# Optimization experiments

Measured on AMD Instinct MI355X. Metric: run time of the kernel, lower is better.

Reference implementation:

```python
import jax, jax.numpy as jnp
import numpy as np

E = 8        # n_routed_experts
K = 4        # num_experts_per_tok
T = 1024     # tokens
H = 1024     # hidden_size
I = 1408     # moe_intermediate_size


def setup_inputs() -> dict:
    key = jax.random.key(0)
    ks = jax.random.split(key, 6)
    hidden_states = jax.random.normal(ks[0], (T, H), jnp.float32)
    rw = jax.random.uniform(ks[1], (T, K), jnp.float32)
    router_weights = rw / jnp.sum(rw, axis=-1, keepdims=True)  # normalized top-k router weights
    selected_experts = jax.random.randint(ks[2], (T, K), 0, E, jnp.int32)
    gate_w = jax.random.normal(ks[3], (E, H, I), jnp.float32) * (H ** -0.5)  # lecun_normal-ish
    up_w = jax.random.normal(ks[4], (E, H, I), jnp.float32) * (H ** -0.5)
    down_w = jax.random.normal(ks[5], (E, I, H), jnp.float32) * (I ** -0.5)
    return {
        'hidden_states': hidden_states,
        'router_weights': router_weights,
        'gate_w': gate_w,
        'up_w': up_w,
        'down_w': down_w,
        'selected_experts': selected_experts,
    }


def _grouped_matmul(x, w, seg):
    # x: [m, k] tokens sorted by expert; w: [E, k, n]; seg: [m] expert id per row.
    # Grouped GEMM expressed as E masked GEMMs (fixed small loop over experts);
    # a custom kernel would do true variable-group-size grouped GEMM.
    out = jnp.zeros((x.shape[0], w.shape[-1]), x.dtype)
    for e in range(w.shape[0]):
        out = out + jnp.where((seg == e)[:, None], x, jnp.zeros((), x.dtype)) @ w[e]
    return out


def reference(hidden_states, router_weights, gate_w, up_w, down_w, selected_experts):
    t, k = selected_experts.shape
    flat = selected_experts.ravel()                       # [t*k]
    hs = jnp.repeat(hidden_states, k, axis=0)             # [t*k, H]
    sort_idx = jnp.argsort(flat)                          # dispatch: sort tokens by expert
    seg = flat[sort_idx]
    xs = hs[sort_idx]
    gate = _grouped_matmul(xs, gate_w, seg)               # [t*k, I]
    up = _grouped_matmul(xs, up_w, seg)                   # [t*k, I]
    h = jax.nn.silu(gate) * up                            # fused SwiGLU
    down = _grouped_matmul(h, down_w, seg)                # [t*k, H]
    unsort = jnp.argsort(sort_idx)                        # scatter back to token order
    out = down[unsort].reshape(t, k, -1)
    return jnp.sum(out * router_weights[..., None], axis=1)  # weighted combine [t, H]
```

## Files before the change

### kernel.cpp

```cpp
#include <hip/hip_runtime.h>
#include <hip/hip_bf16.h>
#include <cstdint>
#include <cstddef>

#define NE 8
#define NT 1024
#define NK 4
#define NH 1024
#define NI 1408
#define NA (NT * NK)
#define BM 128
#define MAXTILES 40
#define PADSLOTS 5120

typedef short short8 __attribute__((ext_vector_type(8)));
typedef float f32x4 __attribute__((ext_vector_type(4)));
typedef float f4v __attribute__((ext_vector_type(4)));
typedef unsigned short u16;

#define WS_HDR   0
#define WS_SORT  1024
#define WS_XBF   21504
#define WS_GT    2118656
#define WS_UT    25187328
#define WS_DT    48256000
#define WS_HB    71324672

__device__ __forceinline__ u16 f2b(float f) {
  union { float f; uint32_t u; } c; c.f = f;
  uint32_t u = c.u;
  return (u16)((u + 0x7FFFu + ((u >> 16) & 1u)) >> 16);
}

__device__ __forceinline__ void llds16(const void* g, void* l) {
  __builtin_amdgcn_global_load_lds(
      (const __attribute__((address_space(1))) void*)g,
      (__attribute__((address_space(3))) void*)l, 16, 0, 0);
}

__device__ __forceinline__ void transcvt_stripe(const float* __restrict__ src,
                                                u16* __restrict__ dst,
                                                int K, int N, int k0, int n0,
                                                u16* smem, int tid) {
  u16 (*t2)[64][72] = (u16(*)[64][72])smem;
  int r = tid >> 4, c = tid & 15;
  f4v v[2][4];
#pragma unroll
  for (int t = 0; t < 2; ++t)
#pragma unroll
    for (int i = 0; i < 4; ++i)
      v[t][i] = __builtin_nontemporal_load(
          (const f4v*)&src[(size_t)(k0 + r + 16 * i) * N + n0 + t * 64 + c * 4]);
#pragma unroll
  for (int t = 0; t < 2; ++t)
#pragma unroll
    for (int i = 0; i < 4; ++i) {
      ushort4 o;
      o.x = f2b(v[t][i].x); o.y = f2b(v[t][i].y); o.z = f2b(v[t][i].z); o.w = f2b(v[t][i].w);
      *(ushort4*)&t2[t][r + 16 * i][c * 4] = o;
    }
  __syncthreads();
#pragma unroll
  for (int t = 0; t < 2; ++t)
#pragma unroll
    for (int i = 0; i < 2; ++i) {
      int idx = i * 256 + tid;
      int n = idx >> 3, kc = idx & 7;
      u16 o[8];
#pragma unroll
      for (int j = 0; j < 8; ++j) o[j] = t2[t][kc * 8 + j][n];
      *(short8*)&dst[(size_t)(n0 + t * 64 + n) * K + k0 + kc * 8] = *(const short8*)o;
    }
}

__global__ __launch_bounds__(256) void k1_prep(
    const float* __restrict__ gw, const float* __restrict__ uw, const float* __restrict__ dw,
    const float* __restrict__ hs, const int* __restrict__ sel,
    u16* __restrict__ gT, u16* __restrict__ uT, u16* __restrict__ dT, u16* __restrict__ xbf,
    int* __restrict__ hdr, int* __restrict__ sorted, float* __restrict__ outz) {
  int tid = threadIdx.x;
  int y = blockIdx.y;
  if (y == 24) {
    for (int i = blockIdx.x * 256 + tid; i * 4 < NT * NH; i += 176 * 256) {
      f4v v = __builtin_nontemporal_load((const f4v*)&hs[i * 4]);
      ushort4 o;
      o.x = f2b(v.x); o.y = f2b(v.y); o.z = f2b(v.z); o.w = f2b(v.w);
      *(ushort4*)&xbf[i * 4] = o;
    }
    return;
  }
  if (y == 25) {
    int x = blockIdx.x;
    if (x >= 1 && x <= 64) {
      int base = (x - 1) * 16384;
      f4v z = {0.f, 0.f, 0.f, 0.f};
#pragma unroll
      for (int i = 0; i < 16; ++i)
        *(f4v*)&outz[base + (i * 256 + tid) * 4] = z;
      return;
    }
    if (x != 0) return;
    __shared__ int cnt[NE], fill[NE], poff_s[NE + 1];
    if (tid < NE) { cnt[tid] = 0; fill[tid] = 0; }
    __syncthreads();
    for (int i = tid; i < NA; i += 256) atomicAdd(&cnt[sel[i]], 1);
    __syncthreads();
    if (tid == 0) {
      int off = 0, nt = 0;
      for (int e = 0; e < NE; ++e) {
        poff_s[e] = off;
        int tiles = (cnt[e] + BM - 1) / BM;
        for (int j = 0; j < tiles; ++j) { hdr[32 + nt] = e; hdr[80 + nt] = off + j * BM; ++nt; }
        off += tiles * BM;
      }
      poff_s[NE] = off;
      hdr[17] = nt;
      for (int e = 0; e < NE; ++e) hdr[e] = cnt[e];
      for (int e = 0; e <= NE; ++e) hdr[8 + e] = poff_s[e];
    }
    __syncthreads();
    for (int i = tid; i < PADSLOTS; i += 256) sorted[i] = -1;
    __syncthreads();
    for (int i = tid; i < NA; i += 256) {
      int e = sel[i];
      int p = atomicAdd(&fill[e], 1);
      sorted[poff_s[e] + p] = i;
    }
    return;
  }
  __shared__ u16 smem[2 * 64 * 72];
  if (y < 16) {
    int tensor = y >> 3, e = y & 7;
    const float* src = ((tensor == 0) ? gw : uw) + (size_t)e * NH * NI;
    u16* dst = ((tensor == 0) ? gT : uT) + (size_t)e * NH * NI;
    int nb = blockIdx.x % 11, kb = blockIdx.x / 11;
    transcvt_stripe(src, dst, NH, NI, kb * 64, nb * 128, smem, tid);
  } else {
    int e = y - 16;
    const float* src = dw + (size_t)e * NI * NH;
    u16* dst = dT + (size_t)e * NI * NH;
    int nb = blockIdx.x % 8, kb = blockIdx.x / 8;
    transcvt_stripe(src, dst, NI, NH, kb * 64, nb * 128, smem, tid);
  }
}

__global__ __launch_bounds__(256, 2) void k2_gemm1(
    const u16* __restrict__ xbf, const u16* __restrict__ gT, const u16* __restrict__ uT,
    u16* __restrict__ hbuf, const int* __restrict__ hdr, const int* __restrict__ sorted) {
  __shared__ u16 smem[24576];
  int b = blockIdx.x;
  int tid = threadIdx.x;

  int tile = b % 40;
  if (tile >= hdr[17]) return;
  int e = hdr[32 + tile];
  int slot0 = hdr[80 + tile];
  int n0 = (b / 40) * 128;

  u16* sA  = smem;
  u16* sBg = smem + 8192;
  u16* sBu = smem + 16384;

  const u16* aptr[4];
  for (int s = 0; s < 4; ++s) {
    int idx = s * 256 + tid;
    int row = idx >> 3, c = idx & 7;
    int kc = c ^ (row & 7);
    int as = sorted[slot0 + row];
    int trow = (as >= 0) ? (as >> 2) : 0;
    aptr[s] = xbf + (size_t)trow * NH + kc * 8;
  }
  const u16 *bgp[4], *bup[4];
  for (int s = 0; s < 4; ++s) {
    int idx = s * 256 + tid;
    int n = idx >> 3, c = idx & 7;
    int kc = c ^ (n & 7);
    size_t o = ((size_t)e * NI + n0 + n) * NH + kc * 8;
    bgp[s] = gT + o; bup[s] = uT + o;
  }

  int lane = tid & 63, wave = tid >> 6;
  int wm = wave >> 1, wn = wave & 1;
  int l15 = lane & 15, quad = lane >> 4;
  int sw = l15 & 7;

  f32x4 accg[4][4] = {}; f32x4 accu[4][4] = {};

  for (int kt = 0; kt < NH / 64; ++kt) {
    int ko = kt * 64;
    for (int s = 0; s < 4; ++s) llds16(aptr[s] + ko, &sA[(s * 256 + tid) * 8]);
    for (int s = 0; s < 4; ++s) llds16(bgp[s] + ko, &sBg[(s * 256 + tid) * 8]);
    for (int s = 0; s < 4; ++s) llds16(bup[s] + ko, &sBu[(s * 256 + tid) * 8]);
    __syncthreads();
    for (int ks = 0; ks < 2; ++ks) {
      int pos = ((ks * 4 + quad) ^ sw) * 8;
      short8 av[4], bg[4], bu[4];
      for (int mf = 0; mf < 4; ++mf)
        av[mf] = *(const short8*)&sA[(wm * 64 + mf * 16 + l15) * 64 + pos];
      for (int nf = 0; nf < 4; ++nf) {
        bg[nf] = *(const short8*)&sBg[(wn * 64 + nf * 16 + l15) * 64 + pos];
        bu[nf] = *(const short8*)&sBu[(wn * 64 + nf * 16 + l15) * 64 + pos];
      }
      for (int mf = 0; mf < 4; ++mf)
        for (int nf = 0; nf < 4; ++nf) {
          accg[mf][nf] = __builtin_amdgcn_mfma_f32_16x16x32_bf16(av[mf], bg[nf], accg[mf][nf], 0, 0, 0);
          accu[mf][nf] = __builtin_amdgcn_mfma_f32_16x16x32_bf16(av[mf], bu[nf], accu[mf][nf], 0, 0, 0);
        }
    }
    __syncthreads();
  }

  for (int mf = 0; mf < 4; ++mf)
    for (int nf = 0; nf < 4; ++nf)
      for (int r = 0; r < 4; ++r) {
        int row = wm * 64 + mf * 16 + quad * 4 + r;
        int col = n0 + wn * 64 + nf * 16 + l15;
        float g2 = accg[mf][nf][r], u = accu[mf][nf][r];
        float hv = (g2 / (1.f + __expf(-g2))) * u;
        hbuf[(size_t)(slot0 + row) * NI + col] = f2b(hv);
      }
}

__global__ __launch_bounds__(256, 4) void k3_gemm2(
    const u16* __restrict__ hbuf, const u16* __restrict__ dT,
    const float* __restrict__ rw, float* __restrict__ out,
    const int* __restrict__ hdr, const int* __restrict__ sorted) {
  int tile = blockIdx.x;
  if (tile >= hdr[17]) return;
  int e = hdr[32 + tile];
  int slot0 = hdr[80 + tile];
  int n0 = blockIdx.y * 128;
  int tid = threadIdx.x;

  __shared__ u16 sA[128 * 64];
  __shared__ u16 sB[128 * 64];

  const u16 *ap[4], *bp[4];
  for (int s = 0; s < 4; ++s) {
    int idx = s * 256 + tid;
    int r = idx >> 3, c = idx & 7;
    int kc = c ^ (r & 7);
    ap[s] = hbuf + (size_t)(slot0 + r) * NI + kc * 8;
    bp[s] = dT + ((size_t)e * NH + n0 + r) * NI + kc * 8;
  }

  int lane = tid & 63, wave = tid >> 6;
  int wm = wave >> 1, wn = wave & 1;
  int l15 = lane & 15, quad = lane >> 4;
  int sw = l15 & 7;

  f32x4 acc[4][4] = {};

  for (int kt = 0; kt < NI / 64; ++kt) {
    int ko = kt * 64;
    for (int s = 0; s < 4; ++s) llds16(ap[s] + ko, &sA[(s * 256 + tid) * 8]);
    for (int s = 0; s < 4; ++s) llds16(bp[s] + ko, &sB[(s * 256 + tid) * 8]);
    __syncthreads();
    for (int ks = 0; ks < 2; ++ks) {
      int pos = ((ks * 4 + quad) ^ sw) * 8;
      short8 av[4], bv[4];
      for (int mf = 0; mf < 4; ++mf)
        av[mf] = *(const short8*)&sA[(wm * 64 + mf * 16 + l15) * 64 + pos];
      for (int nf = 0; nf < 4; ++nf)
        bv[nf] = *(const short8*)&sB[(wn * 64 + nf * 16 + l15) * 64 + pos];
      for (int mf = 0; mf < 4; ++mf)
        for (int nf = 0; nf < 4; ++nf)
          acc[mf][nf] = __builtin_amdgcn_mfma_f32_16x16x32_bf16(av[mf], bv[nf], acc[mf][nf], 0, 0, 0);
    }
    __syncthreads();
  }

  for (int mf = 0; mf < 4; ++mf) {
    int rowb = wm * 64 + mf * 16 + quad * 4;
    for (int r = 0; r < 4; ++r) {
      int as = sorted[slot0 + rowb + r];
      if (as < 0) continue;
      float w = rw[as];
      float* orow = out + (size_t)(as >> 2) * NH + n0 + wn * 64;
      for (int nf = 0; nf < 4; ++nf)
        atomicAdd(&orow[nf * 16 + l15], w * acc[mf][nf][r]);
    }
  }
}

extern "C" void kernel_launch(void* const* d_in, const int* in_sizes, int n_in,
                              void* d_out, int out_size, void* d_ws, size_t ws_size,
                              hipStream_t stream) {
  const float* hs  = (const float*)d_in[0];
  const float* rw  = (const float*)d_in[1];
  const float* gw  = (const float*)d_in[2];
  const float* uw  = (const float*)d_in[3];
  const float* dw  = (const float*)d_in[4];
  const int*   sel = (const int*)d_in[5];
  float* out = (float*)d_out;

  char* ws = (char*)d_ws;
  int*  hdr    = (int*)(ws + WS_HDR);
  int*  sorted = (int*)(ws + WS_SORT);
  u16*  xbf    = (u16*)(ws + WS_XBF);
  u16*  gT     = (u16*)(ws + WS_GT);
  u16*  uT     = (u16*)(ws + WS_UT);
  u16*  dT     = (u16*)(ws + WS_DT);
  u16*  hb     = (u16*)(ws + WS_HB);

  hipLaunchKernelGGL(k1_prep, dim3(176, 26), dim3(256), 0, stream,
                     gw, uw, dw, hs, sel, gT, uT, dT, xbf, hdr, sorted, out);
  hipLaunchKernelGGL(k2_gemm1, dim3(440), dim3(256), 0, stream,
                     xbf, gT, uT, hb, hdr, sorted);
  hipLaunchKernelGGL(k3_gemm2, dim3(MAXTILES, NH / 128), dim3(256), 0, stream,
                     hb, dT, rw, out, hdr, sorted);
}
```

Before: 243.7 us.

## Overlap down-weight transpose-convert with first grouped GEMM and shrink LDS stride

Moves the down_w fp32-to-bf16 transpose from the prep kernel into extra blocks of the gate/up GEMM kernel, so that conversion can run alongside the first GEMM instead of before it. The prep grid shrinks accordingly. The LDS transpose tile stride also changes from 72 to 66 to alter bank mapping. Risks include the extra blocks competing with GEMM blocks for CUs and bandwidth, and the odd stride possibly misaligning the ushort4 LDS stores.

```diff
diff --git a/kernel.cpp b/kernel.cpp
--- a/kernel.cpp
+++ b/kernel.cpp
@@ -26,6 +26,8 @@
 #define WS_DT    48256000
 #define WS_HB    71324672
 
+#define TSTRIDE 66
+
 __device__ __forceinline__ u16 f2b(float f) {
   union { float f; uint32_t u; } c; c.f = f;
   uint32_t u = c.u;
@@ -42,7 +44,7 @@
                                                 u16* __restrict__ dst,
                                                 int K, int N, int k0, int n0,
                                                 u16* smem, int tid) {
-  u16 (*t2)[64][72] = (u16(*)[64][72])smem;
+  u16 (*t2)[64][TSTRIDE] = (u16(*)[64][TSTRIDE])smem;
   int r = tid >> 4, c = tid & 15;
   f4v v[2][4];
 #pragma unroll
@@ -74,13 +76,13 @@
 }
 
 __global__ __launch_bounds__(256) void k1_prep(
-    const float* __restrict__ gw, const float* __restrict__ uw, const float* __restrict__ dw,
+    const float* __restrict__ gw, const float* __restrict__ uw,
     const float* __restrict__ hs, const int* __restrict__ sel,
-    u16* __restrict__ gT, u16* __restrict__ uT, u16* __restrict__ dT, u16* __restrict__ xbf,
+    u16* __restrict__ gT, u16* __restrict__ uT, u16* __restrict__ xbf,
     int* __restrict__ hdr, int* __restrict__ sorted, float* __restrict__ outz) {
   int tid = threadIdx.x;
   int y = blockIdx.y;
-  if (y == 24) {
+  if (y == 16) {
     for (int i = blockIdx.x * 256 + tid; i * 4 < NT * NH; i += 176 * 256) {
       f4v v = __builtin_nontemporal_load((const f4v*)&hs[i * 4]);
       ushort4 o;
@@ -89,7 +91,7 @@
     }
     return;
   }
-  if (y == 25) {
+  if (y == 17) {
     int x = blockIdx.x;
     if (x >= 1 && x <= 64) {
       int base = (x - 1) * 16384;
@@ -128,28 +130,30 @@
     }
     return;
   }
-  __shared__ u16 smem[2 * 64 * 72];
-  if (y < 16) {
-    int tensor = y >> 3, e = y & 7;
-    const float* src = ((tensor == 0) ? gw : uw) + (size_t)e * NH * NI;
-    u16* dst = ((tensor == 0) ? gT : uT) + (size_t)e * NH * NI;
-    int nb = blockIdx.x % 11, kb = blockIdx.x / 11;
-    transcvt_stripe(src, dst, NH, NI, kb * 64, nb * 128, smem, tid);
-  } else {
-    int e = y - 16;
-    const float* src = dw + (size_t)e * NI * NH;
-    u16* dst = dT + (size_t)e * NI * NH;
-    int nb = blockIdx.x % 8, kb = blockIdx.x / 8;
-    transcvt_stripe(src, dst, NI, NH, kb * 64, nb * 128, smem, tid);
-  }
+  __shared__ u16 smem[2 * 64 * TSTRIDE];
+  int tensor = y >> 3, e = y & 7;
+  const float* src = ((tensor == 0) ? gw : uw) + (size_t)e * NH * NI;
+  u16* dst = ((tensor == 0) ? gT : uT) + (size_t)e * NH * NI;
+  int nb = blockIdx.x % 11, kb = blockIdx.x / 11;
+  transcvt_stripe(src, dst, NH, NI, kb * 64, nb * 128, smem, tid);
 }
 
 __global__ __launch_bounds__(256, 2) void k2_gemm1(
     const u16* __restrict__ xbf, const u16* __restrict__ gT, const u16* __restrict__ uT,
-    u16* __restrict__ hbuf, const int* __restrict__ hdr, const int* __restrict__ sorted) {
+    u16* __restrict__ hbuf, const int* __restrict__ hdr, const int* __restrict__ sorted,
+    const float* __restrict__ dw, u16* __restrict__ dT) {
   __shared__ u16 smem[24576];
   int b = blockIdx.x;
   int tid = threadIdx.x;
+
+  if (b >= 440) {
+    int bb = b - 440;
+    int e = bb / 176, x = bb % 176;
+    int nb = x % 8, kb = x / 8;
+    transcvt_stripe(dw + (size_t)e * NI * NH, dT + (size_t)e * NI * NH,
+                    NI, NH, kb * 64, nb * 128, smem, tid);
+    return;
+  }
 
   int tile = b % 40;
   if (tile >= hdr[17]) return;
@@ -303,10 +307,10 @@
   u16*  dT     = (u16*)(ws + WS_DT);
   u16*  hb     = (u16*)(ws + WS_HB);
 
-  hipLaunchKernelGGL(k1_prep, dim3(176, 26), dim3(256), 0, stream,
-                     gw, uw, dw, hs, sel, gT, uT, dT, xbf, hdr, sorted, out);
-  hipLaunchKernelGGL(k2_gemm1, dim3(440), dim3(256), 0, stream,
-                     xbf, gT, uT, hb, hdr, sorted);
+  hipLaunchKernelGGL(k1_prep, dim3(176, 18), dim3(256), 0, stream,
+                     gw, uw, hs, sel, gT, uT, xbf, hdr, sorted, out);
+  hipLaunchKernelGGL(k2_gemm1, dim3(440 + 1408), dim3(256), 0, stream,
+                     xbf, gT, uT, hb, hdr, sorted, dw, dT);
   hipLaunchKernelGGL(k3_gemm2, dim3(MAXTILES, NH / 128), dim3(256), 0, stream,
                      hb, dT, rw, out, hdr, sorted);
 }
```

Measured after the change: 245.6 us. About the same (+0.8%).

## Pair expert tiles into 256-row blocks with double-buffered LDS and split-K down GEMM

Applied to the files above, without the earlier changes.

Groups consecutive 128-row tiles of the same expert into pairs so each 1024-thread block computes 256 rows, sharing each weight tile load across twice as many tokens. Both GEMMs now double-buffer LDS stages so the next K slice loads during MFMA work, and the down projection splits K in two halves that combine through the existing atomic adds. The transpose scratch stride also changes from 72 to 66. This cuts weight traffic and load latency exposure at the cost of fewer, larger blocks, more LDS per block, and twice the atomics in the second GEMM.

```diff
diff --git a/kernel.cpp b/kernel.cpp
--- a/kernel.cpp
+++ b/kernel.cpp
@@ -11,6 +11,7 @@
 #define NA (NT * NK)
 #define BM 128
 #define MAXTILES 40
+#define MAXPAIRS 24
 #define PADSLOTS 5120
 
 typedef short short8 __attribute__((ext_vector_type(8)));
@@ -26,6 +27,8 @@
 #define WS_DT    48256000
 #define WS_HB    71324672
 
+#define TSTRIDE 66
+
 __device__ __forceinline__ u16 f2b(float f) {
   union { float f; uint32_t u; } c; c.f = f;
   uint32_t u = c.u;
@@ -42,7 +45,7 @@
                                                 u16* __restrict__ dst,
                                                 int K, int N, int k0, int n0,
                                                 u16* smem, int tid) {
-  u16 (*t2)[64][72] = (u16(*)[64][72])smem;
+  u16 (*t2)[64][TSTRIDE] = (u16(*)[64][TSTRIDE])smem;
   int r = tid >> 4, c = tid & 15;
   f4v v[2][4];
 #pragma unroll
@@ -106,15 +109,21 @@
     for (int i = tid; i < NA; i += 256) atomicAdd(&cnt[sel[i]], 1);
     __syncthreads();
     if (tid == 0) {
-      int off = 0, nt = 0;
+      int off = 0, nt = 0, np = 0;
       for (int e = 0; e < NE; ++e) {
         poff_s[e] = off;
         int tiles = (cnt[e] + BM - 1) / BM;
         for (int j = 0; j < tiles; ++j) { hdr[32 + nt] = e; hdr[80 + nt] = off + j * BM; ++nt; }
+        for (int j = 0; j < tiles; j += 2) {
+          hdr[128 + np] = e;
+          hdr[160 + np] = off + j * BM;
+          hdr[192 + np] = (j + 1 < tiles) ? (off + (j + 1) * BM) : -1;
+          ++np;
+        }
         off += tiles * BM;
       }
       poff_s[NE] = off;
-      hdr[17] = nt;
+      hdr[17] = nt; hdr[18] = np;
       for (int e = 0; e < NE; ++e) hdr[e] = cnt[e];
       for (int e = 0; e <= NE; ++e) hdr[8 + e] = poff_s[e];
     }
@@ -128,7 +137,7 @@
     }
     return;
   }
-  __shared__ u16 smem[2 * 64 * 72];
+  __shared__ u16 smem[2 * 64 * TSTRIDE];
   if (y < 16) {
     int tensor = y >> 3, e = y & 7;
     const float* src = ((tensor == 0) ? gw : uw) + (size_t)e * NH * NI;
@@ -144,65 +153,76 @@
   }
 }
 
-__global__ __launch_bounds__(256, 2) void k2_gemm1(
+__global__ __launch_bounds__(1024, 4) void k2_gemm1(
     const u16* __restrict__ xbf, const u16* __restrict__ gT, const u16* __restrict__ uT,
     u16* __restrict__ hbuf, const int* __restrict__ hdr, const int* __restrict__ sorted) {
-  __shared__ u16 smem[24576];
+  __shared__ u16 smem[65536];
   int b = blockIdx.x;
+  int p = b / 11, n0 = (b % 11) * 128;
+  if (p >= hdr[18]) return;
+  int e = hdr[128 + p], slotA = hdr[160 + p], slotB = hdr[192 + p];
   int tid = threadIdx.x;
 
-  int tile = b % 40;
-  if (tile >= hdr[17]) return;
-  int e = hdr[32 + tile];
-  int slot0 = hdr[80 + tile];
-  int n0 = (b / 40) * 128;
-
-  u16* sA  = smem;
-  u16* sBg = smem + 8192;
-  u16* sBu = smem + 16384;
-
-  const u16* aptr[4];
-  for (int s = 0; s < 4; ++s) {
-    int idx = s * 256 + tid;
+  const u16* aptr[2];
+#pragma unroll
+  for (int s = 0; s < 2; ++s) {
+    int idx = s * 1024 + tid;
     int row = idx >> 3, c = idx & 7;
     int kc = c ^ (row & 7);
-    int as = sorted[slot0 + row];
+    int srow = (row < 128) ? (slotA + row) : (slotB >= 0 ? slotB + row - 128 : 0);
+    int as = sorted[srow];
     int trow = (as >= 0) ? (as >> 2) : 0;
     aptr[s] = xbf + (size_t)trow * NH + kc * 8;
   }
-  const u16 *bgp[4], *bup[4];
-  for (int s = 0; s < 4; ++s) {
-    int idx = s * 256 + tid;
-    int n = idx >> 3, c = idx & 7;
-    int kc = c ^ (n & 7);
-    size_t o = ((size_t)e * NI + n0 + n) * NH + kc * 8;
-    bgp[s] = gT + o; bup[s] = uT + o;
-  }
+  {
+  }
+  int bn = tid >> 3, bc = tid & 7;
+  int bkc = bc ^ (bn & 7);
+  size_t bo = ((size_t)e * NI + n0 + bn) * NH + bkc * 8;
+  const u16* bgp = gT + bo;
+  const u16* bup = uT + bo;
 
   int lane = tid & 63, wave = tid >> 6;
-  int wm = wave >> 1, wn = wave & 1;
+  int wm = wave >> 2, wn = wave & 3;
   int l15 = lane & 15, quad = lane >> 4;
   int sw = l15 & 7;
 
-  f32x4 accg[4][4] = {}; f32x4 accu[4][4] = {};
-
-  for (int kt = 0; kt < NH / 64; ++kt) {
-    int ko = kt * 64;
-    for (int s = 0; s < 4; ++s) llds16(aptr[s] + ko, &sA[(s * 256 + tid) * 8]);
-    for (int s = 0; s < 4; ++s) llds16(bgp[s] + ko, &sBg[(s * 256 + tid) * 8]);
-    for (int s = 0; s < 4; ++s) llds16(bup[s] + ko, &sBu[(s * 256 + tid) * 8]);
-    __syncthreads();
+  f32x4 accg[4][2] = {}; f32x4 accu[4][2] = {};
+
+#define K2_STAGE(BUF, KT)                                                     \
+  {                                                                           \
+    int ko_ = (KT) * 64;                                                      \
+    u16* base_ = smem + (BUF) * 32768;                                        \
+    llds16(aptr[0] + ko_, base_ + tid * 8);                                   \
+    llds16(aptr[1] + ko_, base_ + (1024 + tid) * 8);                          \
+    llds16(bgp + ko_, base_ + 16384 + tid * 8);                               \
+    llds16(bup + ko_, base_ + 24576 + tid * 8);                               \
+  }
+
+  K2_STAGE(0, 0);
+  __syncthreads();
+  for (int kt = 0; kt < 16; ++kt) {
+    int cur = kt & 1;
+    if (kt < 15) K2_STAGE(cur ^ 1, kt + 1);
+    const u16* sA  = smem + cur * 32768;
+    const u16* sBg = sA + 16384;
+    const u16* sBu = sA + 24576;
+#pragma unroll
     for (int ks = 0; ks < 2; ++ks) {
       int pos = ((ks * 4 + quad) ^ sw) * 8;
-      short8 av[4], bg[4], bu[4];
+      short8 av[4], bg[2], bu[2];
+#pragma unroll
       for (int mf = 0; mf < 4; ++mf)
         av[mf] = *(const short8*)&sA[(wm * 64 + mf * 16 + l15) * 64 + pos];
-      for (int nf = 0; nf < 4; ++nf) {
-        bg[nf] = *(const short8*)&sBg[(wn * 64 + nf * 16 + l15) * 64 + pos];
-        bu[nf] = *(const short8*)&sBu[(wn * 64 + nf * 16 + l15) * 64 + pos];
+#pragma unroll
+      for (int nf = 0; nf < 2; ++nf) {
+        bg[nf] = *(const short8*)&sBg[(wn * 32 + nf * 16 + l15) * 64 + pos];
+        bu[nf] = *(const short8*)&sBu[(wn * 32 + nf * 16 + l15) * 64 + pos];
       }
+#pragma unroll
       for (int mf = 0; mf < 4; ++mf)
-        for (int nf = 0; nf < 4; ++nf) {
+#pragma unroll
+        for (int nf = 0; nf < 2; ++nf) {
           accg[mf][nf] = __builtin_amdgcn_mfma_f32_16x16x32_bf16(av[mf], bg[nf], accg[mf][nf], 0, 0, 0);
           accu[mf][nf] = __builtin_amdgcn_mfma_f32_16x16x32_bf16(av[mf], bu[nf], accu[mf][nf], 0, 0, 0);
         }
@@ -210,77 +230,108 @@
     __syncthreads();
   }
 
+#pragma unroll
   for (int mf = 0; mf < 4; ++mf)
-    for (int nf = 0; nf < 4; ++nf)
-      for (int r = 0; r < 4; ++r) {
-        int row = wm * 64 + mf * 16 + quad * 4 + r;
-        int col = n0 + wn * 64 + nf * 16 + l15;
+#pragma unroll
+    for (int r = 0; r < 4; ++r) {
+      int row = wm * 64 + mf * 16 + quad * 4 + r;
+      int slot = (row < 128) ? (slotA + row) : (slotB >= 0 ? slotB + row - 128 : -1);
+      if (slot < 0) continue;
+#pragma unroll
+      for (int nf = 0; nf < 2; ++nf) {
+        int col = n0 + wn * 32 + nf * 16 + l15;
         float g2 = accg[mf][nf][r], u = accu[mf][nf][r];
         float hv = (g2 / (1.f + __expf(-g2))) * u;
-        hbuf[(size_t)(slot0 + row) * NI + col] = f2b(hv);
+        hbuf[(size_t)slot * NI + col] = f2b(hv);
       }
-}
-
-__global__ __launch_bounds__(256, 4) void k3_gemm2(
+    }
+#undef K2_STAGE
+}
+
+__global__ __launch_bounds__(1024, 4) void k3_gemm2(
     const u16* __restrict__ hbuf, const u16* __restrict__ dT,
     const float* __restrict__ rw, float* __restrict__ out,
     const int* __restrict__ hdr, const int* __restrict__ sorted) {
-  int tile = blockIdx.x;
-  if (tile >= hdr[17]) return;
-  int e = hdr[32 + tile];
-  int slot0 = hdr[80 + tile];
-  int n0 = blockIdx.y * 128;
+  __shared__ u16 smem[49152];
+  int b = blockIdx.x;
+  int p = b >> 4, r16 = b & 15;
+  int n0 = (r16 & 7) * 128, kh = r16 >> 3;
+  if (p >= hdr[18]) return;
+  int e = hdr[128 + p], slotA = hdr[160 + p], slotB = hdr[192 + p];
   int tid = threadIdx.x;
 
-  __shared__ u16 sA[128 * 64];
-  __shared__ u16 sB[128 * 64];
-
-  const u16 *ap[4], *bp[4];
-  for (int s = 0; s < 4; ++s) {
-    int idx = s * 256 + tid;
-    int r = idx >> 3, c = idx & 7;
-    int kc = c ^ (r & 7);
-    ap[s] = hbuf + (size_t)(slot0 + r) * NI + kc * 8;
-    bp[s] = dT + ((size_t)e * NH + n0 + r) * NI + kc * 8;
-  }
+  const u16* aptr[2];
+#pragma unroll
+  for (int s = 0; s < 2; ++s) {
+    int idx = s * 1024 + tid;
+    int row = idx >> 3, c = idx & 7;
+    int kc = c ^ (row & 7);
+    int slot = (row < 128) ? (slotA + row) : (slotB >= 0 ? slotB + row - 128 : 0);
+    aptr[s] = hbuf + (size_t)slot * NI + kc * 8;
+  }
+  int bn = tid >> 3, bc = tid & 7;
+  int bkc = bc ^ (bn & 7);
+  const u16* bp = dT + ((size_t)e * NH + n0 + bn) * NI + bkc * 8;
 
   int lane = tid & 63, wave = tid >> 6;
-  int wm = wave >> 1, wn = wave & 1;
+  int wm = wave >> 2, wn = wave & 3;
   int l15 = lane & 15, quad = lane >> 4;
   int sw = l15 & 7;
 
-  f32x4 acc[4][4] = {};
-
-  for (int kt = 0; kt < NI / 64; ++kt) {
-    int ko = kt * 64;
-    for (int s = 0; s < 4; ++s) llds16(ap[s] + ko, &sA[(s * 256 + tid) * 8]);
-    for (int s = 0; s < 4; ++s) llds16(bp[s] + ko, &sB[(s * 256 + tid) * 8]);
-    __syncthreads();
+  f32x4 acc[4][2] = {};
+
+#define K3_STAGE(BUF, KT)                                                     \
+  {                                                                           \
+    int ko_ = (KT) * 64;                                                      \
+    u16* base_ = smem + (BUF) * 24576;                                        \
+    llds16(aptr[0] + ko_, base_ + tid * 8);                                   \
+    llds16(aptr[1] + ko_, base_ + (1024 + tid) * 8);                          \
+    llds16(bp + ko_, base_ + 16384 + tid * 8);                                \
+  }
+
+  int kt0 = kh * 11;
+  K3_STAGE(0, kt0);
+  __syncthreads();
+  for (int ki = 0; ki < 11; ++ki) {
+    int cur = ki & 1;
+    if (ki < 10) K3_STAGE(cur ^ 1, kt0 + ki + 1);
+    const u16* sA = smem + cur * 24576;
+    const u16* sB = sA + 16384;
+#pragma unroll
     for (int ks = 0; ks < 2; ++ks) {
       int pos = ((ks * 4 + quad) ^ sw) * 8;
-      short8 av[4], bv[4];
+      short8 av[4], bv[2];
+#pragma unroll
       for (int mf = 0; mf < 4; ++mf)
         av[mf] = *(const short8*)&sA[(wm * 64 + mf * 16 + l15) * 64 + pos];
-      for (int nf = 0; nf < 4; ++nf)
-        bv[nf] = *(const short8*)&sB[(wn * 64 + nf * 16 + l15) * 64 + pos];
+#pragma unroll
+      for (int nf = 0; nf < 2; ++nf)
+        bv[nf] = *(const short8*)&sB[(wn * 32 + nf * 16 + l15) * 64 + pos];
+#pragma unroll
       for (int mf = 0; mf < 4; ++mf)
-        for (int nf = 0; nf < 4; ++nf)
+#pragma unroll
+        for (int nf = 0; nf < 2; ++nf)
           acc[mf][nf] = __builtin_amdgcn_mfma_f32_16x16x32_bf16(av[mf], bv[nf], acc[mf][nf], 0, 0, 0);
     }
     __syncthreads();
   }
 
-  for (int mf = 0; mf < 4; ++mf) {
-    int rowb = wm * 64 + mf * 16 + quad * 4;
+#pragma unroll
+  for (int mf = 0; mf < 4; ++mf)
+#pragma unroll
     for (int r = 0; r < 4; ++r) {
-      int as = sorted[slot0 + rowb + r];
+      int row = wm * 64 + mf * 16 + quad * 4 + r;
+      int slot = (row < 128) ? (slotA + row) : (slotB >= 0 ? slotB + row - 128 : -1);
+      if (slot < 0) continue;
+      int as = sorted[slot];
       if (as < 0) continue;
       float w = rw[as];
-      float* orow = out + (size_t)(as >> 2) * NH + n0 + wn * 64;
-      for (int nf = 0; nf < 4; ++nf)
+      float* orow = out + (size_t)(as >> 2) * NH + n0 + wn * 32;
+#pragma unroll
+      for (int nf = 0; nf < 2; ++nf)
         atomicAdd(&orow[nf * 16 + l15], w * acc[mf][nf][r]);
     }
-  }
+#undef K3_STAGE
 }
 
 extern "C" void kernel_launch(void* const* d_in, const int* in_sizes, int n_in,
@@ -305,8 +356,8 @@
 
   hipLaunchKernelGGL(k1_prep, dim3(176, 26), dim3(256), 0, stream,
                      gw, uw, dw, hs, sel, gT, uT, dT, xbf, hdr, sorted, out);
-  hipLaunchKernelGGL(k2_gemm1, dim3(440), dim3(256), 0, stream,
+  hipLaunchKernelGGL(k2_gemm1, dim3(MAXPAIRS * 11), dim3(1024), 0, stream,
                      xbf, gT, uT, hb, hdr, sorted);
-  hipLaunchKernelGGL(k3_gemm2, dim3(MAXTILES, NH / 128), dim3(256), 0, stream,
+  hipLaunchKernelGGL(k3_gemm2, dim3(MAXPAIRS * 16), dim3(1024), 0, stream,
                      hb, dT, rw, out, hdr, sorted);
 }
```

Measured after the change: 248.6 us. 1.02x slower.

## Restructure down-projection GEMM into paired M-tiles with split-K and 1024-thread blocks

Applied to the files above, without the earlier changes.

The down-projection kernel now has each 1024-thread block process a pair of 128-row tiles of the same expert (256 rows), a 128-column output slice and half of the K dimension. The two K-halves are combined through the existing atomic adds into the output. Each B tile loaded into LDS is reused across twice as many rows, and the split-K raises the block count so more CUs stay busy. The cost is twice as many atomic adds, possible wasted work on odd tile counts, and a change of the transpose LDS padding stride from 72 to 66, which may alter bank conflicts.

```diff
diff --git a/kernel.cpp b/kernel.cpp
--- a/kernel.cpp
+++ b/kernel.cpp
@@ -11,6 +11,7 @@
 #define NA (NT * NK)
 #define BM 128
 #define MAXTILES 40
+#define MAXPAIRS 24
 #define PADSLOTS 5120
 
 typedef short short8 __attribute__((ext_vector_type(8)));
@@ -26,6 +27,8 @@
 #define WS_DT    48256000
 #define WS_HB    71324672
 
+#define TSTRIDE 66
+
 __device__ __forceinline__ u16 f2b(float f) {
   union { float f; uint32_t u; } c; c.f = f;
   uint32_t u = c.u;
@@ -42,7 +45,7 @@
                                                 u16* __restrict__ dst,
                                                 int K, int N, int k0, int n0,
                                                 u16* smem, int tid) {
-  u16 (*t2)[64][72] = (u16(*)[64][72])smem;
+  u16 (*t2)[64][TSTRIDE] = (u16(*)[64][TSTRIDE])smem;
   int r = tid >> 4, c = tid & 15;
   f4v v[2][4];
 #pragma unroll
@@ -106,15 +109,21 @@
     for (int i = tid; i < NA; i += 256) atomicAdd(&cnt[sel[i]], 1);
     __syncthreads();
     if (tid == 0) {
-      int off = 0, nt = 0;
+      int off = 0, nt = 0, np = 0;
       for (int e = 0; e < NE; ++e) {
         poff_s[e] = off;
         int tiles = (cnt[e] + BM - 1) / BM;
         for (int j = 0; j < tiles; ++j) { hdr[32 + nt] = e; hdr[80 + nt] = off + j * BM; ++nt; }
+        for (int j = 0; j < tiles; j += 2) {
+          hdr[128 + np] = e;
+          hdr[160 + np] = off + j * BM;
+          hdr[192 + np] = (j + 1 < tiles) ? (off + (j + 1) * BM) : -1;
+          ++np;
+        }
         off += tiles * BM;
       }
       poff_s[NE] = off;
-      hdr[17] = nt;
+      hdr[17] = nt; hdr[18] = np;
       for (int e = 0; e < NE; ++e) hdr[e] = cnt[e];
       for (int e = 0; e <= NE; ++e) hdr[8 + e] = poff_s[e];
     }
@@ -128,7 +137,7 @@
     }
     return;
   }
-  __shared__ u16 smem[2 * 64 * 72];
+  __shared__ u16 smem[2 * 64 * TSTRIDE];
   if (y < 16) {
     int tensor = y >> 3, e = y & 7;
     const float* src = ((tensor == 0) ? gw : uw) + (size_t)e * NH * NI;
@@ -221,66 +230,81 @@
       }
 }
 
-__global__ __launch_bounds__(256, 4) void k3_gemm2(
+__global__ __launch_bounds__(1024, 4) void k3_gemm2(
     const u16* __restrict__ hbuf, const u16* __restrict__ dT,
     const float* __restrict__ rw, float* __restrict__ out,
     const int* __restrict__ hdr, const int* __restrict__ sorted) {
-  int tile = blockIdx.x;
-  if (tile >= hdr[17]) return;
-  int e = hdr[32 + tile];
-  int slot0 = hdr[80 + tile];
-  int n0 = blockIdx.y * 128;
+  __shared__ u16 smem[24576];
+  int b = blockIdx.x;
+  int p = b >> 4, r16 = b & 15;
+  int n0 = (r16 & 7) * 128, kh = r16 >> 3;
+  if (p >= hdr[18]) return;
+  int e = hdr[128 + p], slotA = hdr[160 + p], slotB = hdr[192 + p];
   int tid = threadIdx.x;
 
-  __shared__ u16 sA[128 * 64];
-  __shared__ u16 sB[128 * 64];
-
-  const u16 *ap[4], *bp[4];
-  for (int s = 0; s < 4; ++s) {
-    int idx = s * 256 + tid;
-    int r = idx >> 3, c = idx & 7;
-    int kc = c ^ (r & 7);
-    ap[s] = hbuf + (size_t)(slot0 + r) * NI + kc * 8;
-    bp[s] = dT + ((size_t)e * NH + n0 + r) * NI + kc * 8;
-  }
+  const u16* aptr[2];
+#pragma unroll
+  for (int s = 0; s < 2; ++s) {
+    int idx = s * 1024 + tid;
+    int row = idx >> 3, c = idx & 7;
+    int kc = c ^ (row & 7);
+    int slot = (row < 128) ? (slotA + row) : (slotB >= 0 ? slotB + row - 128 : 0);
+    aptr[s] = hbuf + (size_t)slot * NI + kc * 8;
+  }
+  int bn = tid >> 3, bc = tid & 7;
+  int bkc = bc ^ (bn & 7);
+  const u16* bp = dT + ((size_t)e * NH + n0 + bn) * NI + bkc * 8;
 
   int lane = tid & 63, wave = tid >> 6;
-  int wm = wave >> 1, wn = wave & 1;
+  int wm = wave >> 2, wn = wave & 3;
   int l15 = lane & 15, quad = lane >> 4;
   int sw = l15 & 7;
 
-  f32x4 acc[4][4] = {};
-
-  for (int kt = 0; kt < NI / 64; ++kt) {
-    int ko = kt * 64;
-    for (int s = 0; s < 4; ++s) llds16(ap[s] + ko, &sA[(s * 256 + tid) * 8]);
-    for (int s = 0; s < 4; ++s) llds16(bp[s] + ko, &sB[(s * 256 + tid) * 8]);
-    __syncthreads();
+  f32x4 acc[4][2] = {};
+
+  int kt0 = kh * 11;
+  for (int ki = 0; ki < 11; ++ki) {
+    int ko = (kt0 + ki) * 64;
+    llds16(aptr[0] + ko, &smem[tid * 8]);
+    llds16(aptr[1] + ko, &smem[(1024 + tid) * 8]);
+    llds16(bp + ko, &smem[16384 + tid * 8]);
+    __syncthreads();
+    const u16* sA = smem;
+    const u16* sB = smem + 16384;
+#pragma unroll
     for (int ks = 0; ks < 2; ++ks) {
       int pos = ((ks * 4 + quad) ^ sw) * 8;
-      short8 av[4], bv[4];
+      short8 av[4], bv[2];
+#pragma unroll
       for (int mf = 0; mf < 4; ++mf)
         av[mf] = *(const short8*)&sA[(wm * 64 + mf * 16 + l15) * 64 + pos];
-      for (int nf = 0; nf < 4; ++nf)
-        bv[nf] = *(const short8*)&sB[(wn * 64 + nf * 16 + l15) * 64 + pos];
+#pragma unroll
+      for (int nf = 0; nf < 2; ++nf)
+        bv[nf] = *(const short8*)&sB[(wn * 32 + nf * 16 + l15) * 64 + pos];
+#pragma unroll
       for (int mf = 0; mf < 4; ++mf)
-        for (int nf = 0; nf < 4; ++nf)
+#pragma unroll
+        for (int nf = 0; nf < 2; ++nf)
           acc[mf][nf] = __builtin_amdgcn_mfma_f32_16x16x32_bf16(av[mf], bv[nf], acc[mf][nf], 0, 0, 0);
     }
     __syncthreads();
   }
 
-  for (int mf = 0; mf < 4; ++mf) {
-    int rowb = wm * 64 + mf * 16 + quad * 4;
+#pragma unroll
+  for (int mf = 0; mf < 4; ++mf)
+#pragma unroll
     for (int r = 0; r < 4; ++r) {
-      int as = sorted[slot0 + rowb + r];
+      int row = wm * 64 + mf * 16 + quad * 4 + r;
+      int slot = (row < 128) ? (slotA + row) : (slotB >= 0 ? slotB + row - 128 : -1);
+      if (slot < 0) continue;
+      int as = sorted[slot];
       if (as < 0) continue;
       float w = rw[as];
-      float* orow = out + (size_t)(as >> 2) * NH + n0 + wn * 64;
-      for (int nf = 0; nf < 4; ++nf)
+      float* orow = out + (size_t)(as >> 2) * NH + n0 + wn * 32;
+#pragma unroll
+      for (int nf = 0; nf < 2; ++nf)
         atomicAdd(&orow[nf * 16 + l15], w * acc[mf][nf][r]);
     }
-  }
 }
 
 extern "C" void kernel_launch(void* const* d_in, const int* in_sizes, int n_in,
@@ -307,6 +331,6 @@
                      gw, uw, dw, hs, sel, gT, uT, dT, xbf, hdr, sorted, out);
   hipLaunchKernelGGL(k2_gemm1, dim3(440), dim3(256), 0, stream,
                      xbf, gT, uT, hb, hdr, sorted);
-  hipLaunchKernelGGL(k3_gemm2, dim3(MAXTILES, NH / 128), dim3(256), 0, stream,
+  hipLaunchKernelGGL(k3_gemm2, dim3(MAXPAIRS * 16), dim3(1024), 0, stream,
                      hb, dT, rw, out, hdr, sorted);
 }
```

Result: slower. 262.0 us (+7.5%).
